# Kernel optimization log

Hardware: AMD Instinct MI355X
Metric: run time of the kernel (lower is better)

## Reference

```python
import jax, jax.numpy as jnp
import numpy as np

B, N, H, HD = 32, 256, 6, 32            # windows, tokens/window (16x16), heads, head_dim
C = H * HD                               # dim = 192
TOPK_IN, TOPK_OUT = 64, 32               # incoming pfa topk, num_topk[layer_id]
NBIAS = (2 * 16 - 1) ** 2                # relative-position bias table size = 961
SCALE = HD ** -0.5
EPS = 1e-20


def setup_inputs() -> dict:
    key = jax.random.key(0)
    ks = jax.random.split(key, 7)
    qkvp = jax.random.normal(ks[0], (B, N, 4 * C), dtype=jnp.float32)
    pfa_values = jax.random.uniform(ks[1], (B, H, N, TOPK_IN), dtype=jnp.float32)
    pfa_index = jax.random.randint(ks[2], (B, H, N, TOPK_IN), 0, N, dtype=jnp.int64)
    rpi = jax.random.randint(ks[3], (N, N), 0, NBIAS, dtype=jnp.int64)
    rpb_table = 0.02 * jax.random.normal(ks[4], (NBIAS, H), dtype=jnp.float32)
    proj_w = 0.02 * jax.random.normal(ks[5], (C, C), dtype=jnp.float32)
    proj_b = jnp.zeros((C,), dtype=jnp.float32)
    return {"qkvp": qkvp, "pfa_values": pfa_values, "pfa_index": pfa_index,
            "rpi": rpi, "rpb_table": rpb_table, "proj_w": proj_w, "proj_b": proj_b}


def _gather_rows(x, idx):
    # x: [b, h, n, d], idx: [b, h, n, t] -> [b, h, n, t, d] = x[b, h, idx[b,h,n,t], :]
    return jnp.take_along_axis(x[:, :, None, :, :], idx[..., None], axis=3)


def reference(qkvp, pfa_values, pfa_index, rpi, rpb_table, proj_w, proj_b):
    b_, n, c4 = qkvp.shape
    c = c4 // 4
    hd = c // H
    qkvp = qkvp.reshape(b_, n, 4, H, hd).transpose(2, 0, 3, 1, 4)  # [4, b, h, n, hd]
    q, k, v, v_lepe = qkvp[0], qkvp[1], qkvp[2], qkvp[3]
    q = q * SCALE

    # sparse QK^T over gathered keys: attn[b,h,i,t] = <q[b,h,i], k[b,h,idx[b,h,i,t]]>
    k_sel = _gather_rows(k, pfa_index)                      # [b, h, n, TOPK_IN, hd]
    attn = jnp.einsum('bhnd,bhntd->bhnt', q, k_sel)

    # relative position bias, gathered along the sparse key index
    rpb = rpb_table[rpi.reshape(-1)].reshape(n, n, H).transpose(2, 0, 1)  # [h, n, n]
    bias = jnp.take_along_axis(jnp.broadcast_to(rpb[None], (b_, H, n, n)),
                               pfa_index, axis=-1)           # [b, h, n, TOPK_IN]
    attn = attn + bias

    attn = jax.nn.softmax(attn, axis=-1)

    # progressive focusing: modulate by previous attn values and renormalize
    attn = attn * pfa_values
    denom = attn.sum(axis=-1, keepdims=True)
    attn = (attn + EPS) / (denom + EPS)

    # prune to self.topk = TOPK_OUT entries and remap indices
    topv, topi = jax.lax.top_k(attn, TOPK_OUT)               # [b, h, n, TOPK_OUT]
    new_index = jnp.take_along_axis(pfa_index, topi, axis=-1)

    # sparse attn @ V over gathered values, plus LePE residual
    v_sel = _gather_rows(v, new_index)                       # [b, h, n, TOPK_OUT, hd]
    x = jnp.einsum('bhnt,bhntd->bhnd', topv, v_sel) + v_lepe
    x = x.transpose(0, 2, 1, 3).reshape(b_, n, c)
    x = x @ proj_w.T + proj_b
    return x, topv, new_index
```

## Files before the change

kernel.cpp:

```cpp
#include <hip/hip_runtime.h>

#define B_    32
#define N_    256
#define H_    6
#define HD_   32
#define C_    192
#define C4_   768
#define TKIN  64
#define TKOUT 32
#define GAP32 4u

__global__ __launch_bounds__(256) void attn_topk_kernel(
    const float* __restrict__ qkvp,
    const float* __restrict__ pfa_values,
    const int*   __restrict__ pfa_index,
    const int*   __restrict__ rpi,
    const float* __restrict__ rpb_table,
    float* __restrict__ x_pre,
    float* __restrict__ out_topv,
    float* __restrict__ out_nidx)
{
    const int lane  = threadIdx.x & 63;
    const int wslot = threadIdx.x >> 6;

    const int n  = blockIdx.x;
    const int x  = n & 7;
    const int r  = n >> 3;
    const int bq = r / 384;
    const int wb = r - bq * 384;
    const int b  = x * 4 + bq;
    const int row = b * (H_ * N_) + wb * 4 + wslot;

    const int rem = row - b * (H_ * N_);
    const int h   = rem / N_;
    const int i   = rem - h * N_;

    const int row_off = row * TKIN;
    const int idx  = pfa_index[row_off + lane];
    const float pv = pfa_values[row_off + lane];

    __shared__ uint2  s_pk[4][64];
    __shared__ float  s_k32[4][64];
    __shared__ double s_k64[4][64];
    __shared__ float  s_a[4][TKOUT];
    __shared__ int    s_i[4][TKOUT];

    const float* qp = qkvp + (size_t)(b * N_ + i) * C4_ + h * HD_;
    const float* kp = qkvp + (size_t)(b * N_ + idx) * C4_ + C_ + h * HD_;
    const float bias = rpb_table[rpi[i * N_ + idx] * H_ + h];

    double acc64 = 0.0;
    for (int d = 0; d < HD_; ++d)
        acc64 = fma((double)qp[d], (double)kp[d], acc64);
    acc64 = acc64 * 0.17677669529663687 + (double)bias;
    const double okey = exp(acc64) * (double)pv;

    double dsum = okey;
    #pragma unroll
    for (int s = 32; s; s >>= 1) dsum += __shfl_xor(dsum, s);

    union { double d; unsigned long long u; } ou; ou.d = okey;
    const unsigned long long ob = ou.u;
    const unsigned long long myK = (ob & ~63ull) | (unsigned long long)(63 - lane);
    s_pk[wslot][lane] = make_uint2((unsigned)myK, (unsigned)(myK >> 32));

    int rank = 0;
    #pragma unroll
    for (int j = 0; j < 64; ++j) {
        const uint2 kj = s_pk[wslot][j];
        const unsigned long long K =
            ((unsigned long long)kj.y << 32) | (unsigned long long)kj.x;
        rank += (K > myK);
    }

    const unsigned otop = (unsigned)(ob >> 32);
    const int sorted = __builtin_amdgcn_ds_permute(rank << 2, (int)otop);
    const int nxt    = __shfl_down(sorted, 1);
    const unsigned gap = (unsigned)sorted - (unsigned)nxt;
    const bool nearf = (lane < 63) && (gap <= GAP32);

    float outval;
    if (__any(nearf)) {
        float acc;
        {
            #pragma clang fp contract(off)
            const float SC = 0.17677669529663687f;
            acc = 0.f;
            for (int d = 0; d < HD_; ++d) {
                const float qd   = qp[d] * SC;
                const float prod = qd * kp[d];
                acc = acc + prod;
            }
            acc = acc + bias;
        }
        float m = acc;
        #pragma unroll
        for (int s = 32; s; s >>= 1) m = fmaxf(m, __shfl_xor(m, s));
        float e;
        {
            #pragma clang fp contract(off)
            const float t = acc - m;
            e = (float)exp((double)t);
        }
        float ssum;
        {
            #pragma clang fp contract(off)
            float y = e, r2 = e;
            #pragma unroll
            for (int k = 1; k < 8; ++k) { y = __shfl_down(y, 8); r2 = r2 + y; }
            const float t1 = r2 + __shfl_xor(r2, 1);
            const float t2 = t1 + __shfl_xor(t1, 2);
            const float t3 = t2 + __shfl_xor(t2, 4);
            ssum = __shfl(t3, 0);
        }
        float w;
        {
            #pragma clang fp contract(off)
            const float s32 = e / ssum;
            w = s32 * pv;
        }
        float denom;
        {
            #pragma clang fp contract(off)
            float y = w, r2 = w;
            #pragma unroll
            for (int k = 1; k < 8; ++k) { y = __shfl_down(y, 8); r2 = r2 + y; }
            const float t1 = r2 + __shfl_xor(r2, 1);
            const float t2 = t1 + __shfl_xor(t1, 2);
            const float t3 = t2 + __shfl_xor(t2, 4);
            denom = __shfl(t3, 0);
        }
        float a32;
        {
            #pragma clang fp contract(off)
            a32 = (w + 1e-20f) / (denom + 1e-20f);
        }

        s_k32[wslot][lane] = a32;
        s_k64[wslot][lane] = okey;

        rank = 0;
        #pragma unroll
        for (int j = 0; j < 64; ++j) {
            const float  kj32 = s_k32[wslot][j];
            const double kj64 = s_k64[wslot][j];
            const bool tie  = (kj32 == a32);
            const bool lt64 = (kj64 < okey);
            const bool gt64 = (kj64 > okey);
            const bool eq64 = (kj64 == okey);
            const bool before = tie ? (lt64 || (eq64 && j < lane))
                                    : (gt64 || (eq64 && kj32 > a32));
            rank += before;
        }
        outval = a32;
    } else {
        outval = (float)(okey / dsum);
    }

    if (rank < TKOUT) {
        const size_t obase = (size_t)row * TKOUT + rank;
        out_topv[obase] = outval;
        out_nidx[obase] = (float)idx;
        s_a[wslot][rank] = outval;
        s_i[wslot][rank] = idx;
    }

    const int d    = lane & 31;
    const int half = lane >> 5;
    float xd = 0.f;
    #pragma unroll
    for (int s16 = 0; s16 < 16; ++s16) {
        const int sI = half * 16 + s16;
        const float av = s_a[wslot][sI];
        const int   vi = s_i[wslot][sI];
        xd += av * qkvp[(size_t)(b * N_ + vi) * C4_ + 2 * C_ + h * HD_ + d];
    }
    xd += __shfl_xor(xd, 32);
    if (half == 0) {
        const float lepe = qkvp[(size_t)(b * N_ + i) * C4_ + 3 * C_ + h * HD_ + d];
        x_pre[(size_t)(b * N_ + i) * C_ + h * HD_ + d] = xd + lepe;
    }
}

#define TB_ 8
__global__ __launch_bounds__(192) void proj_kernel(
    const float* __restrict__ x_pre,
    const float* __restrict__ w,
    const float* __restrict__ bias,
    float* __restrict__ out)
{
    __shared__ float xs[TB_ * C_];
    const int o    = threadIdx.x;
    const int tok0 = blockIdx.x * TB_;

    #pragma unroll
    for (int r = 0; r < TB_; ++r)
        xs[r * C_ + o] = x_pre[(size_t)(tok0 + r) * C_ + o];
    __syncthreads();

    float accv[TB_];
    #pragma unroll
    for (int t = 0; t < TB_; ++t) accv[t] = 0.f;

    const float* wrow = w + (size_t)o * C_;
    for (int c = 0; c < C_; c += 4) {
        const float4 wv = *(const float4*)(wrow + c);
        #pragma unroll
        for (int t = 0; t < TB_; ++t) {
            const float4 xv = *(const float4*)(&xs[t * C_ + c]);
            accv[t] += xv.x * wv.x + xv.y * wv.y + xv.z * wv.z + xv.w * wv.w;
        }
    }
    const float bo = bias[o];
    #pragma unroll
    for (int t = 0; t < TB_; ++t)
        out[(size_t)(tok0 + t) * C_ + o] = accv[t] + bo;
}

extern "C" void kernel_launch(void* const* d_in, const int* in_sizes, int n_in,
                              void* d_out, int out_size, void* d_ws, size_t ws_size,
                              hipStream_t stream) {
    const float* qkvp       = (const float*)d_in[0];
    const float* pfa_values = (const float*)d_in[1];
    const int*   pfa_index  = (const int*)d_in[2];
    const int*   rpi        = (const int*)d_in[3];
    const float* rpb_table  = (const float*)d_in[4];
    const float* proj_w     = (const float*)d_in[5];
    const float* proj_b     = (const float*)d_in[6];

    float* out = (float*)d_out;
    float* out_x    = out;
    float* out_topv = out + (size_t)B_ * N_ * C_;
    float* out_nidx = out_topv + (size_t)B_ * H_ * N_ * TKOUT;

    float* x_pre = (float*)d_ws;

    const int rows = B_ * H_ * N_;
    attn_topk_kernel<<<rows / 4, 256, 0, stream>>>(
        qkvp, pfa_values, pfa_index, rpi, rpb_table, x_pre, out_topv, out_nidx);

    const int ntok = B_ * N_;
    proj_kernel<<<ntok / TB_, 192, 0, stream>>>(x_pre, proj_w, proj_b, out_x);
}
```

Measured before the change: 114.4 us.

## Stage per-head K tile in LDS and loop each block over 64 query rows

Each block now loads the full 256x32 K slice for one (window, head) into padded shared memory once, then iterates 16 times over groups of four query rows, reading gathered keys from LDS instead of scattered global loads. The grid shrinks from 12288 to 768 blocks. This is meant to cut redundant global K traffic from the random gather. In exchange it uses about 34KB of LDS per block and gives far fewer, longer blocks, which may lower occupancy and latency hiding. The unaligned row-wise reads of the padded Kl array may also cause LDS bank conflicts.

```diff
diff --git a/kernel.cpp b/kernel.cpp
--- a/kernel.cpp
+++ b/kernel.cpp
@@ -22,163 +22,182 @@
 {
     const int lane  = threadIdx.x & 63;
     const int wslot = threadIdx.x >> 6;
+    const int tid   = threadIdx.x;
 
     const int n  = blockIdx.x;
     const int x  = n & 7;
     const int r  = n >> 3;
-    const int bq = r / 384;
-    const int wb = r - bq * 384;
-    const int b  = x * 4 + bq;
-    const int row = b * (H_ * N_) + wb * 4 + wslot;
-
-    const int rem = row - b * (H_ * N_);
-    const int h   = rem / N_;
-    const int i   = rem - h * N_;
-
-    const int row_off = row * TKIN;
-    const int idx  = pfa_index[row_off + lane];
-    const float pv = pfa_values[row_off + lane];
-
+    const int b  = x * 4 + r / 24;
+    const int rr = r % 24;
+    const int h  = rr >> 2;
+    const int quarter = rr & 3;
+
+    __shared__ float  Kl[256][33];
     __shared__ uint2  s_pk[4][64];
     __shared__ float  s_k32[4][64];
     __shared__ double s_k64[4][64];
     __shared__ float  s_a[4][TKOUT];
     __shared__ int    s_i[4][TKOUT];
 
-    const float* qp = qkvp + (size_t)(b * N_ + i) * C4_ + h * HD_;
-    const float* kp = qkvp + (size_t)(b * N_ + idx) * C4_ + C_ + h * HD_;
-    const float bias = rpb_table[rpi[i * N_ + idx] * H_ + h];
-
-    double acc64 = 0.0;
-    for (int d = 0; d < HD_; ++d)
-        acc64 = fma((double)qp[d], (double)kp[d], acc64);
-    acc64 = acc64 * 0.17677669529663687 + (double)bias;
-    const double okey = exp(acc64) * (double)pv;
-
-    double dsum = okey;
-    #pragma unroll
-    for (int s = 32; s; s >>= 1) dsum += __shfl_xor(dsum, s);
-
-    union { double d; unsigned long long u; } ou; ou.d = okey;
-    const unsigned long long ob = ou.u;
-    const unsigned long long myK = (ob & ~63ull) | (unsigned long long)(63 - lane);
-    s_pk[wslot][lane] = make_uint2((unsigned)myK, (unsigned)(myK >> 32));
-
-    int rank = 0;
-    #pragma unroll
-    for (int j = 0; j < 64; ++j) {
-        const uint2 kj = s_pk[wslot][j];
-        const unsigned long long K =
-            ((unsigned long long)kj.y << 32) | (unsigned long long)kj.x;
-        rank += (K > myK);
+    {
+        const int rrow = tid >> 3;
+        const int col  = (tid & 7) * 4;
+        #pragma unroll
+        for (int c = 0; c < 8; ++c) {
+            const int krow = c * 32 + rrow;
+            const float4 v = *(const float4*)(
+                qkvp + (size_t)(b * N_ + krow) * C4_ + C_ + h * HD_ + col);
+            Kl[krow][col + 0] = v.x;
+            Kl[krow][col + 1] = v.y;
+            Kl[krow][col + 2] = v.z;
+            Kl[krow][col + 3] = v.w;
+        }
     }
-
-    const unsigned otop = (unsigned)(ob >> 32);
-    const int sorted = __builtin_amdgcn_ds_permute(rank << 2, (int)otop);
-    const int nxt    = __shfl_down(sorted, 1);
-    const unsigned gap = (unsigned)sorted - (unsigned)nxt;
-    const bool nearf = (lane < 63) && (gap <= GAP32);
-
-    float outval;
-    if (__any(nearf)) {
-        float acc;
-        {
-            #pragma clang fp contract(off)
-            const float SC = 0.17677669529663687f;
-            acc = 0.f;
-            for (int d = 0; d < HD_; ++d) {
-                const float qd   = qp[d] * SC;
-                const float prod = qd * kp[d];
-                acc = acc + prod;
-            }
-            acc = acc + bias;
-        }
-        float m = acc;
-        #pragma unroll
-        for (int s = 32; s; s >>= 1) m = fmaxf(m, __shfl_xor(m, s));
-        float e;
-        {
-            #pragma clang fp contract(off)
-            const float t = acc - m;
-            e = (float)exp((double)t);
-        }
-        float ssum;
-        {
-            #pragma clang fp contract(off)
-            float y = e, r2 = e;
+    __syncthreads();
+
+    for (int it = 0; it < 16; ++it) {
+        const int i   = quarter * 64 + it * 4 + wslot;
+        const int row = (b * H_ + h) * N_ + i;
+
+        const int row_off = row * TKIN;
+        const int idx  = pfa_index[row_off + lane];
+        const float pv = pfa_values[row_off + lane];
+
+        const float* qp = qkvp + (size_t)(b * N_ + i) * C4_ + h * HD_;
+        const float bias = rpb_table[rpi[i * N_ + idx] * H_ + h];
+        const float* kl = &Kl[idx][0];
+
+        double acc64 = 0.0;
+        for (int d = 0; d < HD_; ++d)
+            acc64 = fma((double)qp[d], (double)kl[d], acc64);
+        acc64 = acc64 * 0.17677669529663687 + (double)bias;
+        const double okey = exp(acc64) * (double)pv;
+
+        double dsum = okey;
+        #pragma unroll
+        for (int s = 32; s; s >>= 1) dsum += __shfl_xor(dsum, s);
+
+        union { double d; unsigned long long u; } ou; ou.d = okey;
+        const unsigned long long ob = ou.u;
+        const unsigned long long myK = (ob & ~63ull) | (unsigned long long)(63 - lane);
+        s_pk[wslot][lane] = make_uint2((unsigned)myK, (unsigned)(myK >> 32));
+
+        int rank = 0;
+        #pragma unroll
+        for (int j = 0; j < 64; ++j) {
+            const uint2 kj = s_pk[wslot][j];
+            const unsigned long long K =
+                ((unsigned long long)kj.y << 32) | (unsigned long long)kj.x;
+            rank += (K > myK);
+        }
+
+        const unsigned otop = (unsigned)(ob >> 32);
+        const int sorted = __builtin_amdgcn_ds_permute(rank << 2, (int)otop);
+        const int nxt    = __shfl_down(sorted, 1);
+        const unsigned gap = (unsigned)sorted - (unsigned)nxt;
+        const bool nearf = (lane < 63) && (gap <= GAP32);
+
+        float outval;
+        if (__any(nearf)) {
+            float acc;
+            {
+                #pragma clang fp contract(off)
+                const float SC = 0.17677669529663687f;
+                acc = 0.f;
+                for (int d = 0; d < HD_; ++d) {
+                    const float qd   = qp[d] * SC;
+                    const float prod = qd * kl[d];
+                    acc = acc + prod;
+                }
+                acc = acc + bias;
+            }
+            float m = acc;
             #pragma unroll
-            for (int k = 1; k < 8; ++k) { y = __shfl_down(y, 8); r2 = r2 + y; }
-            const float t1 = r2 + __shfl_xor(r2, 1);
-            const float t2 = t1 + __shfl_xor(t1, 2);
-            const float t3 = t2 + __shfl_xor(t2, 4);
-            ssum = __shfl(t3, 0);
-        }
-        float w;
-        {
-            #pragma clang fp contract(off)
-            const float s32 = e / ssum;
-            w = s32 * pv;
-        }
-        float denom;
-        {
-            #pragma clang fp contract(off)
-            float y = w, r2 = w;
+            for (int s = 32; s; s >>= 1) m = fmaxf(m, __shfl_xor(m, s));
+            float e;
+            {
+                #pragma clang fp contract(off)
+                const float t = acc - m;
+                e = (float)exp((double)t);
+            }
+            float ssum;
+            {
+                #pragma clang fp contract(off)
+                float y = e, r2 = e;
+                #pragma unroll
+                for (int k = 1; k < 8; ++k) { y = __shfl_down(y, 8); r2 = r2 + y; }
+                const float t1 = r2 + __shfl_xor(r2, 1);
+                const float t2 = t1 + __shfl_xor(t1, 2);
+                const float t3 = t2 + __shfl_xor(t2, 4);
+                ssum = __shfl(t3, 0);
+            }
+            float w;
+            {
+                #pragma clang fp contract(off)
+                const float s32 = e / ssum;
+                w = s32 * pv;
+            }
+            float denom;
+            {
+                #pragma clang fp contract(off)
+                float y = w, r2 = w;
+                #pragma unroll
+                for (int k = 1; k < 8; ++k) { y = __shfl_down(y, 8); r2 = r2 + y; }
+                const float t1 = r2 + __shfl_xor(r2, 1);
+                const float t2 = t1 + __shfl_xor(t1, 2);
+                const float t3 = t2 + __shfl_xor(t2, 4);
+                denom = __shfl(t3, 0);
+            }
+            float a32;
+            {
+                #pragma clang fp contract(off)
+                a32 = (w + 1e-20f) / (denom + 1e-20f);
+            }
+
+            s_k32[wslot][lane] = a32;
+            s_k64[wslot][lane] = okey;
+
+            rank = 0;
             #pragma unroll
-            for (int k = 1; k < 8; ++k) { y = __shfl_down(y, 8); r2 = r2 + y; }
-            const float t1 = r2 + __shfl_xor(r2, 1);
-            const float t2 = t1 + __shfl_xor(t1, 2);
-            const float t3 = t2 + __shfl_xor(t2, 4);
-            denom = __shfl(t3, 0);
-        }
-        float a32;
-        {
-            #pragma clang fp contract(off)
-            a32 = (w + 1e-20f) / (denom + 1e-20f);
-        }
-
-        s_k32[wslot][lane] = a32;
-        s_k64[wslot][lane] = okey;
-
-        rank = 0;
-        #pragma unroll
-        for (int j = 0; j < 64; ++j) {
-            const float  kj32 = s_k32[wslot][j];
-            const double kj64 = s_k64[wslot][j];
-            const bool tie  = (kj32 == a32);
-            const bool lt64 = (kj64 < okey);
-            const bool gt64 = (kj64 > okey);
-            const bool eq64 = (kj64 == okey);
-            const bool before = tie ? (lt64 || (eq64 && j < lane))
-                                    : (gt64 || (eq64 && kj32 > a32));
-            rank += before;
-        }
-        outval = a32;
-    } else {
-        outval = (float)(okey / dsum);
-    }
-
-    if (rank < TKOUT) {
-        const size_t obase = (size_t)row * TKOUT + rank;
-        out_topv[obase] = outval;
-        out_nidx[obase] = (float)idx;
-        s_a[wslot][rank] = outval;
-        s_i[wslot][rank] = idx;
-    }
-
-    const int d    = lane & 31;
-    const int half = lane >> 5;
-    float xd = 0.f;
-    #pragma unroll
-    for (int s16 = 0; s16 < 16; ++s16) {
-        const int sI = half * 16 + s16;
-        const float av = s_a[wslot][sI];
-        const int   vi = s_i[wslot][sI];
-        xd += av * qkvp[(size_t)(b * N_ + vi) * C4_ + 2 * C_ + h * HD_ + d];
-    }
-    xd += __shfl_xor(xd, 32);
-    if (half == 0) {
-        const float lepe = qkvp[(size_t)(b * N_ + i) * C4_ + 3 * C_ + h * HD_ + d];
-        x_pre[(size_t)(b * N_ + i) * C_ + h * HD_ + d] = xd + lepe;
+            for (int j = 0; j < 64; ++j) {
+                const float  kj32 = s_k32[wslot][j];
+                const double kj64 = s_k64[wslot][j];
+                const bool tie  = (kj32 == a32);
+                const bool lt64 = (kj64 < okey);
+                const bool gt64 = (kj64 > okey);
+                const bool eq64 = (kj64 == okey);
+                const bool before = tie ? (lt64 || (eq64 && j < lane))
+                                        : (gt64 || (eq64 && kj32 > a32));
+                rank += before;
+            }
+            outval = a32;
+        } else {
+            outval = (float)(okey / dsum);
+        }
+
+        if (rank < TKOUT) {
+            const size_t obase = (size_t)row * TKOUT + rank;
+            out_topv[obase] = outval;
+            out_nidx[obase] = (float)idx;
+            s_a[wslot][rank] = outval;
+            s_i[wslot][rank] = idx;
+        }
+
+        const int d    = lane & 31;
+        const int half = lane >> 5;
+        float xd = 0.f;
+        #pragma unroll
+        for (int s16 = 0; s16 < 16; ++s16) {
+            const int sI = half * 16 + s16;
+            const float av = s_a[wslot][sI];
+            const int   vi = s_i[wslot][sI];
+            xd += av * qkvp[(size_t)(b * N_ + vi) * C4_ + 2 * C_ + h * HD_ + d];
+        }
+        xd += __shfl_xor(xd, 32);
+        if (half == 0) {
+            const float lepe = qkvp[(size_t)(b * N_ + i) * C4_ + 3 * C_ + h * HD_ + d];
+            x_pre[(size_t)(b * N_ + i) * C_ + h * HD_ + d] = xd + lepe;
+        }
     }
 }
 
@@ -235,8 +254,7 @@
 
     float* x_pre = (float*)d_ws;
 
-    const int rows = B_ * H_ * N_;
-    attn_topk_kernel<<<rows / 4, 256, 0, stream>>>(
+    attn_topk_kernel<<<768, 256, 0, stream>>>(
         qkvp, pfa_values, pfa_index, rpi, rpb_table, x_pre, out_topv, out_nidx);
 
     const int ntok = B_ * N_;
```

Measured after the change: 116.0 us. Within noise of the previous version (+1.3%).
